# Performance work log

Measured on AMD Instinct MI355X. Metric: run time of the kernel, lower is better.

The kernel has to match this reference:

```python
import jax, jax.numpy as jnp
import numpy as np

D_MODEL = 512
N_HEADS = 8
HEAD_DIM = D_MODEL // N_HEADS
NEG_INF = -1e9


def setup_inputs() -> dict:
    key = jax.random.key(0)
    ks = jax.random.split(key, 12)
    B, N, M = 8, 2048, 2048
    inp = {
        'query': jax.random.normal(ks[0], (B, D_MODEL, N), jnp.float32),
        'key': jax.random.normal(ks[1], (B, D_MODEL, M), jnp.float32),
        'value': jax.random.normal(ks[2], (B, D_MODEL, M), jnp.float32),
        'query_mask': jnp.ones((B, N), jnp.float32),
        'key_value_mask': jnp.ones((B, M), jnp.float32),
        # Conv1d(d_model, d_model, kernel_size=1) == pointwise linear: W [out, in], b [out]
        'Wq': jax.random.normal(ks[3], (D_MODEL, D_MODEL), jnp.float32) / np.sqrt(D_MODEL),
        'bq': jax.random.normal(ks[4], (D_MODEL,), jnp.float32) * 0.01,
        'Wk': jax.random.normal(ks[5], (D_MODEL, D_MODEL), jnp.float32) / np.sqrt(D_MODEL),
        'bk': jax.random.normal(ks[6], (D_MODEL,), jnp.float32) * 0.01,
        'Wv': jax.random.normal(ks[7], (D_MODEL, D_MODEL), jnp.float32) / np.sqrt(D_MODEL),
        'bv': jax.random.normal(ks[8], (D_MODEL,), jnp.float32) * 0.01,
        'Wm': jax.random.normal(ks[9], (D_MODEL, D_MODEL), jnp.float32) / np.sqrt(D_MODEL),
        'bm': jax.random.normal(ks[10], (D_MODEL,), jnp.float32) * 0.01,
    }
    return inp


def _pointwise(W, b, x):
    # Conv1d k=1 over [B, C_in, N] -> [B, C_out, N]
    return jnp.einsum('oi,bin->bon', W, x) + b[None, :, None]


def reference(query, key, value, query_mask, key_value_mask,
              Wq, bq, Wk, bk, Wv, bv, Wm, bm):
    B = query.shape[0]
    N = query.shape[2]
    M = key.shape[2]
    # project and split heads: [B, head_dim, n_heads, seq]
    q = _pointwise(Wq, bq, query).reshape(B, HEAD_DIM, N_HEADS, N)
    k = _pointwise(Wk, bk, key).reshape(B, HEAD_DIM, N_HEADS, M)
    v = _pointwise(Wv, bv, value).reshape(B, HEAD_DIM, N_HEADS, M)
    # scores [B, H, N, M], scaled by sqrt(head_dim) (query.shape[1] post-split)
    scores = jnp.einsum('bdhn,bdhm->bhnm', q, k) / jnp.sqrt(jnp.float32(HEAD_DIM))
    # dual mask: outer product of key_value_mask [B,1,1,M] and query_mask [B,1,N,1]
    mask = key_value_mask[:, None, None, :] * query_mask[:, None, :, None]
    scores = jnp.where(mask > 0, scores, NEG_INF)
    prob = jax.nn.softmax(scores, axis=-1)  # [B, H, N, M]
    x = jnp.einsum('bhnm,bdhm->bdhn', prob, v)  # [B, head_dim, H, N]
    out = _pointwise(Wm, bm, x.reshape(B, D_MODEL, N))
    return out
```

## Files before the change

kernel.cpp:

```cpp
#include <hip/hip_runtime.h>


typedef _Float16 f16;
typedef _Float16 f16x4 __attribute__((ext_vector_type(4)));
typedef _Float16 f16x8 __attribute__((ext_vector_type(8)));
typedef float f32x4 __attribute__((ext_vector_type(4)));

#define D_MODEL 512
#define HD 64
#define SEQ 2048

__global__ __launch_bounds__(256) void k_transpose(
    const float* __restrict__ q, const float* __restrict__ k, const float* __restrict__ v,
    f16* __restrict__ XT)
{
  __shared__ __align__(16) f16 Ts[64][72];
  int t = threadIdx.x;
  int nt = blockIdx.x, ct = blockIdx.y, z = blockIdx.z;
  int src = z >> 3, b = z & 7;
  const float* S = (src == 0) ? q : (src == 1) ? k : v;
  {
    int cr = t >> 2, ns = t & 3;
    const float* p = S + ((size_t)b * D_MODEL + ct * 64 + cr) * SEQ + nt * 64 + ns * 16;
    f32x4 a0 = *(const f32x4*)(p);
    f32x4 a1 = *(const f32x4*)(p + 4);
    f32x4 a2 = *(const f32x4*)(p + 8);
    f32x4 a3 = *(const f32x4*)(p + 12);
    f16x8 h0, h1;
#pragma unroll
    for (int j = 0; j < 4; ++j) { h0[j] = (f16)a0[j]; h0[4 + j] = (f16)a1[j]; h1[j] = (f16)a2[j]; h1[4 + j] = (f16)a3[j]; }
    *(f16x8*)&Ts[cr][ns * 16] = h0;
    *(f16x8*)&Ts[cr][ns * 16 + 8] = h1;
  }
  __syncthreads();
  {
    int nr = t >> 2, cs = t & 3;
    f16x8 h0, h1;
#pragma unroll
    for (int j = 0; j < 8; ++j) h0[j] = Ts[cs * 16 + j][nr];
#pragma unroll
    for (int j = 0; j < 8; ++j) h1[j] = Ts[cs * 16 + 8 + j][nr];
    f16* dst = XT + (((size_t)z) * SEQ + nt * 64 + nr) * D_MODEL + ct * 64 + cs * 16;
    *(f16x8*)dst = h0;
    *(f16x8*)(dst + 8) = h1;
  }
}

__global__ __launch_bounds__(256) void k_wconv(
    const float* __restrict__ Wq, const float* __restrict__ Wk, const float* __restrict__ Wv,
    const float* __restrict__ Wm, f16* __restrict__ W3, f16* __restrict__ Wmh)
{
  int idx = blockIdx.x * 256 + threadIdx.x;
  if (idx < 262144) {
    W3[idx] = (f16)Wq[idx];
    W3[262144 + idx] = (f16)Wk[idx];
    W3[524288 + idx] = (f16)Wv[idx];
    int o = idx >> 9, c = idx & 511;
    int h = c & 7, d = c >> 3;
    Wmh[((size_t)h * 512 + o) * 64 + d] = (f16)Wm[idx];
  }
}

__global__ __launch_bounds__(256, 2) void k_proj(
    const f16* __restrict__ W3, const float* __restrict__ bq, const float* __restrict__ bk,
    const float* __restrict__ bv, const f16* __restrict__ XT,
    f16* __restrict__ Qt, f16* __restrict__ Kt, f16* __restrict__ Vh)
{
  __shared__ __align__(16) char smem[34816];
  f16 (*As)[40] = (f16(*)[40])smem;
  f16 (*Bs)[40] = (f16(*)[40])(smem + 10240);
  f16 (*Ls)[136] = (f16(*)[136])smem;

  int t = threadIdx.x;
  int proj = blockIdx.z, b = blockIdx.y;
  int ot = blockIdx.x & 3, ntile = blockIdx.x >> 2;
  int w = t >> 6, ln = t & 63, i16 = ln & 15, q4 = ln >> 4;
  int ow = w >> 1, nw = w & 1;

  const f16* Wp = W3 + (size_t)proj * 262144;
  const f16* Xp = XT + ((size_t)proj * 8 + b) * (size_t)SEQ * D_MODEL;

  f32x4 acc[4][4];
#pragma unroll
  for (int x = 0; x < 4; ++x)
#pragma unroll
    for (int y = 0; y < 4; ++y) acc[x][y] = (f32x4){0.f, 0.f, 0.f, 0.f};

  int srow = t >> 1, sseg = t & 1;
  for (int kc = 0; kc < 16; ++kc) {
    __syncthreads();
    const f16* Ap = Wp + ((size_t)(ot * 128 + srow)) * 512 + kc * 32 + sseg * 16;
    *(f32x4*)&As[srow][sseg * 16] = *(const f32x4*)(Ap);
    *(f32x4*)&As[srow][sseg * 16 + 8] = *(const f32x4*)(Ap + 8);
    const f16* Bp = Xp + ((size_t)(ntile * 128 + srow)) * 512 + kc * 32 + sseg * 16;
    *(f32x4*)&Bs[srow][sseg * 16] = *(const f32x4*)(Bp);
    *(f32x4*)&Bs[srow][sseg * 16 + 8] = *(const f32x4*)(Bp + 8);
    __syncthreads();
    f16x8 af[4], bf[4];
#pragma unroll
    for (int x = 0; x < 4; ++x) af[x] = *(const f16x8*)&As[ow * 64 + x * 16 + i16][q4 * 8];
#pragma unroll
    for (int y = 0; y < 4; ++y) bf[y] = *(const f16x8*)&Bs[nw * 64 + y * 16 + i16][q4 * 8];
#pragma unroll
    for (int x = 0; x < 4; ++x)
#pragma unroll
      for (int y = 0; y < 4; ++y)
        acc[x][y] = __builtin_amdgcn_mfma_f32_16x16x32_f16(af[x], bf[y], acc[x][y], 0, 0, 0);
  }

  const float* bias = (proj == 0) ? bq : (proj == 1) ? bk : bv;
  __syncthreads();
#pragma unroll
  for (int x = 0; x < 4; ++x) {
    f32x4 bb = *(const f32x4*)(bias + ot * 128 + ow * 64 + x * 16 + q4 * 4);
#pragma unroll
    for (int y = 0; y < 4; ++y)
#pragma unroll
      for (int r = 0; r < 4; ++r)
        Ls[ow * 64 + x * 16 + q4 * 4 + r][nw * 64 + y * 16 + i16] = (f16)(acc[x][y][r] + bb[r]);
  }
  __syncthreads();
  if (proj < 2) {
    f16* dst = (proj == 0) ? Qt : Kt;
#pragma unroll
    for (int rnd = 0; rnd < 4; ++rnd) {
      int task = rnd * 256 + t;
      int nl = task & 127, h = task >> 7;
      f16x8 g0, g1;
#pragma unroll
      for (int j = 0; j < 8; ++j) g0[j] = Ls[8 * j + h][nl];
#pragma unroll
      for (int j = 0; j < 8; ++j) g1[j] = Ls[8 * (8 + j) + h][nl];
      f16* dp = dst + (((size_t)(b * 8 + h)) * SEQ + ntile * 128 + nl) * HD + ot * 16;
      *(f16x8*)dp = g0;
      *(f16x8*)(dp + 8) = g1;
    }
  } else {
#pragma unroll
    for (int p = 0; p < 8; ++p) {
      int ol = (t >> 4) + 16 * p;
      int ch = t & 15;
      int og = ot * 128 + ol;
      int h = og & 7, d = og >> 3;
      f16* dp = Vh + (((size_t)(b * 8 + h)) * HD + d) * SEQ + ntile * 128 + ch * 8;
      *(f32x4*)dp = *(const f32x4*)&Ls[ol][ch * 8];
    }
  }
}

__global__ __launch_bounds__(256, 2) void k_attn(
    const f16* __restrict__ Qt, const f16* __restrict__ Kt, const f16* __restrict__ Vh,
    const float* __restrict__ qmask, const float* __restrict__ kvmask,
    f16* __restrict__ O)
{
  __shared__ __align__(16) char smem[55552];
  f16 (*Qs)[72] = (f16(*)[72])smem;
  f16 (*Ks)[72] = (f16(*)[72])(smem + 36864);
  f16 (*Vs)[72] = (f16(*)[72])(smem + 46080);
  float* kvb = (float*)(smem + 55296);

  int t = threadIdx.x;
  int bh = blockIdx.x >> 3;
  int b = bh >> 3;
  int n0 = (blockIdx.x & 7) * 256;
  int w = t >> 6, ln = t & 63, i16 = ln & 15, q4 = ln >> 4;

  const f16* Qb = Qt + (size_t)bh * SEQ * HD;
  const f16* Kb = Kt + (size_t)bh * SEQ * HD;
  const f16* Vb = Vh + (size_t)bh * HD * SEQ;

#pragma unroll
  for (int p = 0; p < 8; ++p) {
    int row = (t >> 3) + 32 * p, ch = t & 7;
    *(f32x4*)&Qs[row][ch * 8] = *(const f32x4*)(Qb + ((size_t)(n0 + row)) * HD + ch * 8);
  }
  __syncthreads();
  f16x8 qf[4][2];
#pragma unroll
  for (int nt = 0; nt < 4; ++nt)
#pragma unroll
    for (int kc = 0; kc < 2; ++kc)
      qf[nt][kc] = *(const f16x8*)&Qs[w * 64 + nt * 16 + i16][kc * 32 + q4 * 8];
  float qok[4];
#pragma unroll
  for (int nt = 0; nt < 4; ++nt)
    qok[nt] = qmask[(size_t)b * SEQ + n0 + w * 64 + nt * 16 + i16];

  f32x4 acc_o[4][4];
#pragma unroll
  for (int dt = 0; dt < 4; ++dt)
#pragma unroll
    for (int nt = 0; nt < 4; ++nt) acc_o[dt][nt] = (f32x4){0.f, 0.f, 0.f, 0.f};
  float m_i[4] = {-3e38f, -3e38f, -3e38f, -3e38f};
  float l_i[4] = {0.f, 0.f, 0.f, 0.f};

  for (int it = 0; it < 32; ++it) {
    int m0 = it * 64;
    __syncthreads();
#pragma unroll
    for (int p = 0; p < 2; ++p) {
      int row = (t >> 3) + 32 * p, ch = t & 7;
      *(f32x4*)&Ks[row][ch * 8] = *(const f32x4*)(Kb + ((size_t)(m0 + row)) * HD + ch * 8);
      *(f32x4*)&Vs[row][ch * 8] = *(const f32x4*)(Vb + ((size_t)row) * SEQ + m0 + ch * 8);
    }
    if (t < 64) {
      float kv = kvmask[(size_t)b * SEQ + m0 + t];
      kvb[t] = (kv > 0.f) ? 0.f : -1e9f;
    }
    __syncthreads();

    f16x8 kf[4][2];
#pragma unroll
    for (int mt = 0; mt < 4; ++mt)
#pragma unroll
      for (int kc = 0; kc < 2; ++kc)
        kf[mt][kc] = *(const f16x8*)&Ks[mt * 16 + i16][kc * 32 + q4 * 8];

    f32x4 st[4][4];
#pragma unroll
    for (int mt = 0; mt < 4; ++mt)
#pragma unroll
      for (int nt = 0; nt < 4; ++nt) {
        f32x4 a = (f32x4){0.f, 0.f, 0.f, 0.f};
        a = __builtin_amdgcn_mfma_f32_16x16x32_f16(kf[mt][0], qf[nt][0], a, 0, 0, 0);
        a = __builtin_amdgcn_mfma_f32_16x16x32_f16(kf[mt][1], qf[nt][1], a, 0, 0, 0);
        st[mt][nt] = a;
      }

    f32x4 kvf[4];
#pragma unroll
    for (int mt = 0; mt < 4; ++mt) kvf[mt] = *(const f32x4*)&kvb[mt * 16 + q4 * 4];

    f16x4 pf[4][4];
    float al[4];
#pragma unroll
    for (int nt = 0; nt < 4; ++nt) {
      float mx = -3e38f;
#pragma unroll
      for (int mt = 0; mt < 4; ++mt)
#pragma unroll
        for (int r = 0; r < 4; ++r) {
          float sv = st[mt][nt][r] * 0.125f + kvf[mt][r];
          sv = (qok[nt] > 0.f) ? sv : -1e9f;
          st[mt][nt][r] = sv;
          mx = fmaxf(mx, sv);
        }
      mx = fmaxf(mx, __shfl_xor(mx, 16, 64));
      mx = fmaxf(mx, __shfl_xor(mx, 32, 64));
      float mnew = fmaxf(m_i[nt], mx);
      float alpha = __expf(m_i[nt] - mnew);
      float rsum = 0.f;
#pragma unroll
      for (int mt = 0; mt < 4; ++mt) {
        f16x4 pv;
#pragma unroll
        for (int r = 0; r < 4; ++r) {
          float pe = __expf(st[mt][nt][r] - mnew);
          rsum += pe;
          pv[r] = (f16)pe;
        }
        pf[mt][nt] = pv;
      }
      rsum += __shfl_xor(rsum, 16, 64);
      rsum += __shfl_xor(rsum, 32, 64);
      l_i[nt] = l_i[nt] * alpha + rsum;
      m_i[nt] = mnew;
      al[nt] = alpha;
    }

    f16x4 vf[4][4];
#pragma unroll
    for (int dt = 0; dt < 4; ++dt)
#pragma unroll
      for (int mt = 0; mt < 4; ++mt)
        vf[dt][mt] = *(const f16x4*)&Vs[dt * 16 + i16][mt * 16 + q4 * 4];

#pragma unroll
    for (int dt = 0; dt < 4; ++dt)
#pragma unroll
      for (int nt = 0; nt < 4; ++nt) {
        f32x4 o = acc_o[dt][nt];
        float a = al[nt];
#pragma unroll
        for (int r = 0; r < 4; ++r) o[r] *= a;
#pragma unroll
        for (int mt = 0; mt < 4; ++mt)
          o = __builtin_amdgcn_mfma_f32_16x16x16f16(vf[dt][mt], pf[mt][nt], o, 0, 0, 0);
        acc_o[dt][nt] = o;
      }
  }

  __syncthreads();
  f16 (*Os)[72] = (f16(*)[72])(smem + w * 9216);
#pragma unroll
  for (int nt = 0; nt < 4; ++nt) {
    float inv = 1.f / l_i[nt];
#pragma unroll
    for (int dt = 0; dt < 4; ++dt) {
      f16x4 o4;
#pragma unroll
      for (int r = 0; r < 4; ++r) o4[r] = (f16)(acc_o[dt][nt][r] * inv);
      *(f16x4*)&Os[nt * 16 + i16][dt * 16 + q4 * 4] = o4;
    }
  }
  __syncthreads();
  f16* Ob = O + ((size_t)bh * SEQ + n0 + w * 64) * HD;
#pragma unroll
  for (int p = 0; p < 8; ++p) {
    int row = (ln >> 3) + 8 * p, ch = ln & 7;
    *(f32x4*)(Ob + (size_t)row * HD + ch * 8) = *(const f32x4*)&Os[row][ch * 8];
  }
}

__global__ __launch_bounds__(256, 2) void k_out(
    const f16* __restrict__ Wmh, const float* __restrict__ bm,
    const f16* __restrict__ O, float* __restrict__ out)
{
  __shared__ __align__(16) char smem[20480];
  f16 (*As)[40] = (f16(*)[40])smem;
  f16 (*Bs)[40] = (f16(*)[40])(smem + 10240);

  int t = threadIdx.x;
  int b = blockIdx.y;
  int ot = blockIdx.x & 3, ntile = blockIdx.x >> 2;
  int w = t >> 6, ln = t & 63, i16 = ln & 15, q4 = ln >> 4;
  int ow = w >> 1, nw = w & 1;

  f32x4 acc[4][4];
#pragma unroll
  for (int x = 0; x < 4; ++x)
#pragma unroll
    for (int y = 0; y < 4; ++y) acc[x][y] = (f32x4){0.f, 0.f, 0.f, 0.f};

  int srow = t >> 1, sseg = t & 1;
  for (int ck = 0; ck < 16; ++ck) {
    int h = ck >> 1, dc = ck & 1;
    __syncthreads();
    const f16* Ap = Wmh + ((size_t)h * 512 + ot * 128 + srow) * 64 + dc * 32 + sseg * 16;
    *(f32x4*)&As[srow][sseg * 16] = *(const f32x4*)(Ap);
    *(f32x4*)&As[srow][sseg * 16 + 8] = *(const f32x4*)(Ap + 8);
    const f16* Bp = O + (((size_t)(b * 8 + h)) * SEQ + ntile * 128 + srow) * 64 + dc * 32 + sseg * 16;
    *(f32x4*)&Bs[srow][sseg * 16] = *(const f32x4*)(Bp);
    *(f32x4*)&Bs[srow][sseg * 16 + 8] = *(const f32x4*)(Bp + 8);
    __syncthreads();
    f16x8 af[4], bf[4];
#pragma unroll
    for (int x = 0; x < 4; ++x) af[x] = *(const f16x8*)&As[ow * 64 + x * 16 + i16][q4 * 8];
#pragma unroll
    for (int y = 0; y < 4; ++y) bf[y] = *(const f16x8*)&Bs[nw * 64 + y * 16 + i16][q4 * 8];
#pragma unroll
    for (int x = 0; x < 4; ++x)
#pragma unroll
      for (int y = 0; y < 4; ++y)
        acc[x][y] = __builtin_amdgcn_mfma_f32_16x16x32_f16(af[x], bf[y], acc[x][y], 0, 0, 0);
  }

#pragma unroll
  for (int x = 0; x < 4; ++x) {
    f32x4 bb = *(const f32x4*)(bm + ot * 128 + ow * 64 + x * 16 + q4 * 4);
#pragma unroll
    for (int y = 0; y < 4; ++y)
#pragma unroll
      for (int r = 0; r < 4; ++r) {
        int o_g = ot * 128 + ow * 64 + x * 16 + q4 * 4 + r;
        int n_g = ntile * 128 + nw * 64 + y * 16 + i16;
        out[((size_t)b * 512 + o_g) * SEQ + n_g] = acc[x][y][r] + bb[r];
      }
  }
}

extern "C" void kernel_launch(void* const* d_in, const int* in_sizes, int n_in,
                              void* d_out, int out_size, void* d_ws, size_t ws_size,
                              hipStream_t stream)
{
  const float* query  = (const float*)d_in[0];
  const float* key    = (const float*)d_in[1];
  const float* value  = (const float*)d_in[2];
  const float* qmask  = (const float*)d_in[3];
  const float* kvmask = (const float*)d_in[4];
  const float* Wq = (const float*)d_in[5];
  const float* bq = (const float*)d_in[6];
  const float* Wk = (const float*)d_in[7];
  const float* bk = (const float*)d_in[8];
  const float* Wv = (const float*)d_in[9];
  const float* bv = (const float*)d_in[10];
  const float* Wm = (const float*)d_in[11];
  const float* bm = (const float*)d_in[12];
  float* out = (float*)d_out;

  char* ws = (char*)d_ws;
  f16* XT  = (f16*)(ws);
  f16* Qt  = (f16*)(ws + 50331648);
  f16* Kt  = (f16*)(ws + 67108864);
  f16* Vh  = (f16*)(ws + 83886080);
  f16* Oat = (f16*)(ws);
  f16* W3  = (f16*)(ws + 100663296);
  f16* Wmh = (f16*)(ws + 102236160);

  k_transpose<<<dim3(32, 8, 24), 256, 0, stream>>>(query, key, value, XT);
  k_wconv<<<1024, 256, 0, stream>>>(Wq, Wk, Wv, Wm, W3, Wmh);
  k_proj<<<dim3(64, 8, 3), 256, 0, stream>>>(W3, bq, bk, bv, XT, Qt, Kt, Vh);
  k_attn<<<512, 256, 0, stream>>>(Qt, Kt, Vh, qmask, kvmask, Oat);
  k_out<<<dim3(64, 8), 256, 0, stream>>>(Wmh, bm, Oat, out);
}
```

Before: 367.8 us.

## Shrink attention query tile, fold scale into Q, use exp2 softmax

The attention kernel now processes 128 queries per block instead of 256 (32 per wave). It reuses the Q staging shared memory for K/V and launches 1024 blocks with a higher occupancy hint, aiming to cut per-block LDS and register use so more waves fit per CU. The softmax scale and log2(e) are folded into the Q projection epilogue, the kv mask bias is fed in as the MFMA accumulator init, and exp is replaced by the hardware exp2 instruction. This removes per-element multiply and add work in the inner loop. In exchange K/V tiles are loaded twice as often per query, and Q is stored pre-scaled in fp16, which slightly changes rounding.

```diff
diff --git a/kernel.cpp b/kernel.cpp
--- a/kernel.cpp
+++ b/kernel.cpp
@@ -9,6 +9,8 @@
 #define D_MODEL 512
 #define HD 64
 #define SEQ 2048
+#define QSCL 0.18033688011112042f
+#define KVNEG -1.4426950409e9f
 
 __global__ __launch_bounds__(256) void k_transpose(
     const float* __restrict__ q, const float* __restrict__ k, const float* __restrict__ v,
@@ -109,6 +111,7 @@
   }
 
   const float* bias = (proj == 0) ? bq : (proj == 1) ? bk : bv;
+  float scl = (proj == 0) ? QSCL : 1.0f;
   __syncthreads();
 #pragma unroll
   for (int x = 0; x < 4; ++x) {
@@ -117,7 +120,7 @@
     for (int y = 0; y < 4; ++y)
 #pragma unroll
       for (int r = 0; r < 4; ++r)
-        Ls[ow * 64 + x * 16 + q4 * 4 + r][nw * 64 + y * 16 + i16] = (f16)(acc[x][y][r] + bb[r]);
+        Ls[ow * 64 + x * 16 + q4 * 4 + r][nw * 64 + y * 16 + i16] = (f16)((acc[x][y][r] + bb[r]) * scl);
   }
   __syncthreads();
   if (proj < 2) {
@@ -148,21 +151,21 @@
   }
 }
 
-__global__ __launch_bounds__(256, 2) void k_attn(
+__global__ __launch_bounds__(256, 4) void k_attn(
     const f16* __restrict__ Qt, const f16* __restrict__ Kt, const f16* __restrict__ Vh,
     const float* __restrict__ qmask, const float* __restrict__ kvmask,
     f16* __restrict__ O)
 {
-  __shared__ __align__(16) char smem[55552];
+  __shared__ __align__(16) char smem[18688];
   f16 (*Qs)[72] = (f16(*)[72])smem;
-  f16 (*Ks)[72] = (f16(*)[72])(smem + 36864);
-  f16 (*Vs)[72] = (f16(*)[72])(smem + 46080);
-  float* kvb = (float*)(smem + 55296);
+  f16 (*Ks)[72] = (f16(*)[72])smem;
+  f16 (*Vs)[72] = (f16(*)[72])(smem + 9216);
+  float* kvb = (float*)(smem + 18432);
 
   int t = threadIdx.x;
-  int bh = blockIdx.x >> 3;
+  int bh = blockIdx.x >> 4;
   int b = bh >> 3;
-  int n0 = (blockIdx.x & 7) * 256;
+  int n0 = (blockIdx.x & 15) * 128;
   int w = t >> 6, ln = t & 63, i16 = ln & 15, q4 = ln >> 4;
 
   const f16* Qb = Qt + (size_t)bh * SEQ * HD;
@@ -170,29 +173,29 @@
   const f16* Vb = Vh + (size_t)bh * HD * SEQ;
 
 #pragma unroll
-  for (int p = 0; p < 8; ++p) {
+  for (int p = 0; p < 4; ++p) {
     int row = (t >> 3) + 32 * p, ch = t & 7;
     *(f32x4*)&Qs[row][ch * 8] = *(const f32x4*)(Qb + ((size_t)(n0 + row)) * HD + ch * 8);
   }
   __syncthreads();
-  f16x8 qf[4][2];
-#pragma unroll
-  for (int nt = 0; nt < 4; ++nt)
+  f16x8 qf[2][2];
+#pragma unroll
+  for (int nt = 0; nt < 2; ++nt)
 #pragma unroll
     for (int kc = 0; kc < 2; ++kc)
-      qf[nt][kc] = *(const f16x8*)&Qs[w * 64 + nt * 16 + i16][kc * 32 + q4 * 8];
-  float qok[4];
-#pragma unroll
-  for (int nt = 0; nt < 4; ++nt)
-    qok[nt] = qmask[(size_t)b * SEQ + n0 + w * 64 + nt * 16 + i16];
-
-  f32x4 acc_o[4][4];
+      qf[nt][kc] = *(const f16x8*)&Qs[w * 32 + nt * 16 + i16][kc * 32 + q4 * 8];
+  float qok[2];
+#pragma unroll
+  for (int nt = 0; nt < 2; ++nt)
+    qok[nt] = qmask[(size_t)b * SEQ + n0 + w * 32 + nt * 16 + i16];
+
+  f32x4 acc_o[4][2];
 #pragma unroll
   for (int dt = 0; dt < 4; ++dt)
 #pragma unroll
-    for (int nt = 0; nt < 4; ++nt) acc_o[dt][nt] = (f32x4){0.f, 0.f, 0.f, 0.f};
-  float m_i[4] = {-3e38f, -3e38f, -3e38f, -3e38f};
-  float l_i[4] = {0.f, 0.f, 0.f, 0.f};
+    for (int nt = 0; nt < 2; ++nt) acc_o[dt][nt] = (f32x4){0.f, 0.f, 0.f, 0.f};
+  float m_i[2] = {-3e38f, -3e38f};
+  float l_i[2] = {0.f, 0.f};
 
   for (int it = 0; it < 32; ++it) {
     int m0 = it * 64;
@@ -205,7 +208,7 @@
     }
     if (t < 64) {
       float kv = kvmask[(size_t)b * SEQ + m0 + t];
-      kvb[t] = (kv > 0.f) ? 0.f : -1e9f;
+      kvb[t] = (kv > 0.f) ? 0.f : KVNEG;
     }
     __syncthreads();
 
@@ -215,50 +218,46 @@
 #pragma unroll
       for (int kc = 0; kc < 2; ++kc)
         kf[mt][kc] = *(const f16x8*)&Ks[mt * 16 + i16][kc * 32 + q4 * 8];
-
-    f32x4 st[4][4];
-#pragma unroll
-    for (int mt = 0; mt < 4; ++mt)
-#pragma unroll
-      for (int nt = 0; nt < 4; ++nt) {
-        f32x4 a = (f32x4){0.f, 0.f, 0.f, 0.f};
+    f32x4 kvf[4];
+#pragma unroll
+    for (int mt = 0; mt < 4; ++mt) kvf[mt] = *(const f32x4*)&kvb[mt * 16 + q4 * 4];
+
+    f16x4 pf[4][2];
+    float al[2];
+#pragma unroll
+    for (int nt = 0; nt < 2; ++nt) {
+      f32x4 s[4];
+#pragma unroll
+      for (int mt = 0; mt < 4; ++mt) {
+        f32x4 a = kvf[mt];
         a = __builtin_amdgcn_mfma_f32_16x16x32_f16(kf[mt][0], qf[nt][0], a, 0, 0, 0);
         a = __builtin_amdgcn_mfma_f32_16x16x32_f16(kf[mt][1], qf[nt][1], a, 0, 0, 0);
-        st[mt][nt] = a;
+        s[mt] = a;
       }
-
-    f32x4 kvf[4];
-#pragma unroll
-    for (int mt = 0; mt < 4; ++mt) kvf[mt] = *(const f32x4*)&kvb[mt * 16 + q4 * 4];
-
-    f16x4 pf[4][4];
-    float al[4];
-#pragma unroll
-    for (int nt = 0; nt < 4; ++nt) {
+      bool qz = qok[nt] > 0.f;
       float mx = -3e38f;
 #pragma unroll
       for (int mt = 0; mt < 4; ++mt)
 #pragma unroll
         for (int r = 0; r < 4; ++r) {
-          float sv = st[mt][nt][r] * 0.125f + kvf[mt][r];
-          sv = (qok[nt] > 0.f) ? sv : -1e9f;
-          st[mt][nt][r] = sv;
+          float sv = qz ? s[mt][r] : KVNEG;
+          s[mt][r] = sv;
           mx = fmaxf(mx, sv);
         }
       mx = fmaxf(mx, __shfl_xor(mx, 16, 64));
       mx = fmaxf(mx, __shfl_xor(mx, 32, 64));
       float mnew = fmaxf(m_i[nt], mx);
-      float alpha = __expf(m_i[nt] - mnew);
+      float alpha = __builtin_amdgcn_exp2f(m_i[nt] - mnew);
       float rsum = 0.f;
 #pragma unroll
       for (int mt = 0; mt < 4; ++mt) {
+        float p0 = __builtin_amdgcn_exp2f(s[mt][0] - mnew);
+        float p1 = __builtin_amdgcn_exp2f(s[mt][1] - mnew);
+        float p2 = __builtin_amdgcn_exp2f(s[mt][2] - mnew);
+        float p3 = __builtin_amdgcn_exp2f(s[mt][3] - mnew);
+        rsum += (p0 + p1) + (p2 + p3);
         f16x4 pv;
-#pragma unroll
-        for (int r = 0; r < 4; ++r) {
-          float pe = __expf(st[mt][nt][r] - mnew);
-          rsum += pe;
-          pv[r] = (f16)pe;
-        }
+        pv[0] = (f16)p0; pv[1] = (f16)p1; pv[2] = (f16)p2; pv[3] = (f16)p3;
         pf[mt][nt] = pv;
       }
       rsum += __shfl_xor(rsum, 16, 64);
@@ -278,7 +277,7 @@
 #pragma unroll
     for (int dt = 0; dt < 4; ++dt)
 #pragma unroll
-      for (int nt = 0; nt < 4; ++nt) {
+      for (int nt = 0; nt < 2; ++nt) {
         f32x4 o = acc_o[dt][nt];
         float a = al[nt];
 #pragma unroll
@@ -291,9 +290,9 @@
   }
 
   __syncthreads();
-  f16 (*Os)[72] = (f16(*)[72])(smem + w * 9216);
-#pragma unroll
-  for (int nt = 0; nt < 4; ++nt) {
+  f16 (*Os)[72] = (f16(*)[72])(smem + w * 4608);
+#pragma unroll
+  for (int nt = 0; nt < 2; ++nt) {
     float inv = 1.f / l_i[nt];
 #pragma unroll
     for (int dt = 0; dt < 4; ++dt) {
@@ -304,9 +303,9 @@
     }
   }
   __syncthreads();
-  f16* Ob = O + ((size_t)bh * SEQ + n0 + w * 64) * HD;
-#pragma unroll
-  for (int p = 0; p < 8; ++p) {
+  f16* Ob = O + ((size_t)bh * SEQ + n0 + w * 32) * HD;
+#pragma unroll
+  for (int p = 0; p < 4; ++p) {
     int row = (ln >> 3) + 8 * p, ch = ln & 7;
     *(f32x4*)(Ob + (size_t)row * HD + ch * 8) = *(const f32x4*)&Os[row][ch * 8];
   }
@@ -400,6 +399,6 @@
   k_transpose<<<dim3(32, 8, 24), 256, 0, stream>>>(query, key, value, XT);
   k_wconv<<<1024, 256, 0, stream>>>(Wq, Wk, Wv, Wm, W3, Wmh);
   k_proj<<<dim3(64, 8, 3), 256, 0, stream>>>(W3, bq, bk, bv, XT, Qt, Kt, Vh);
-  k_attn<<<512, 256, 0, stream>>>(Qt, Kt, Vh, qmask, kvmask, Oat);
+  k_attn<<<1024, 256, 0, stream>>>(Qt, Kt, Vh, qmask, kvmask, Oat);
   k_out<<<dim3(64, 8), 256, 0, stream>>>(Wmh, bm, Oat, out);
 }
```

After: 356.1 us. 1.03x faster.
